# Performance work log

Hardware: AMD Instinct MI355X
Metric: run time of the kernel (lower is better)

Reference implementation:

```python
import jax, jax.numpy as jnp
import numpy as np

B, L, C = 32, 8192, 64
LEVELS = 3  # detail kernels 3,5,9 with pads 1,2,4


def _conv1d(x, w, b, pad):
    # x: [B, C, L], w: [O, I, K] (torch Conv1d layout), b: [O]
    y = jax.lax.conv_general_dilated(
        x, w, window_strides=(1,), padding=[(pad, pad)],
        dimension_numbers=('NCH', 'OIH', 'NCH'))
    return y + b[None, :, None]


def _block(xc, w1, b1, w2, b2, pad):
    # Conv1d(k) -> ReLU -> Conv1d(k=1)
    h = jax.nn.relu(_conv1d(xc, w1, b1, pad))
    return _conv1d(h, w2, b2, 0)


def setup_inputs() -> dict:
    key = jax.random.key(0)
    ks = jax.random.split(key, 20)
    s = 0.05  # keep activations stable
    inp = {
        'x': jax.random.normal(ks[0], (B, L, C), jnp.float32),
        'rec_weights': jnp.ones((LEVELS + 1,), jnp.float32) / (LEVELS + 1),
        'trend_w1': jax.random.normal(ks[1], (C, C, 3), jnp.float32) * s,
        'trend_b1': jnp.zeros((C,), jnp.float32),
        'trend_w2': jax.random.normal(ks[2], (C, C, 1), jnp.float32) * s,
        'trend_b2': jnp.zeros((C,), jnp.float32),
    }
    kernels = [3, 5, 9]
    for i, k in enumerate(kernels, start=1):
        inp[f'd{i}_w1'] = jax.random.normal(ks[2 + 2 * i], (C, C, k), jnp.float32) * s
        inp[f'd{i}_b1'] = jnp.zeros((C,), jnp.float32)
        inp[f'd{i}_w2'] = jax.random.normal(ks[3 + 2 * i], (C, C, 1), jnp.float32) * s
        inp[f'd{i}_b2'] = jnp.zeros((C,), jnp.float32)
    return inp


def reference(x, rec_weights,
              trend_w1, trend_b1, trend_w2, trend_b2,
              d1_w1, d1_b1, d1_w2, d1_b2,
              d2_w1, d2_b1, d2_w2, d2_b2,
              d3_w1, d3_b1, d3_w2, d3_b2):
    # component_fusion forward: x [B, L, C] -> [B, L, C]
    xc = jnp.transpose(x, (0, 2, 1))  # [B, C, L]
    trend = _block(xc, trend_w1, trend_b1, trend_w2, trend_b2, 1)
    d1 = _block(xc, d1_w1, d1_b1, d1_w2, d1_b2, 1)   # k=3, pad=1
    d2 = _block(xc, d2_w1, d2_b1, d2_w2, d2_b2, 2)   # k=5, pad=2
    d3 = _block(xc, d3_w1, d3_b1, d3_w2, d3_b2, 4)   # k=9, pad=4
    w = jax.nn.softmax(rec_weights)
    fused = w[0] * trend + w[1] * d1 + w[2] * d2 + w[3] * d3
    return jnp.transpose(fused, (0, 2, 1))
```

## Files before the change

### kernel.cpp

```cpp
#include <hip/hip_runtime.h>


constexpr int Bn = 32, Ln = 8192;
constexpr int NT = 256;
constexpr int HALO = 4;
constexpr int XROWS = NT + 2 * HALO;
constexpr int RS = 72;
constexpr int NSLICE = 24;

using bf16x8 = __attribute__((ext_vector_type(8))) __bf16;
using f32x4  = __attribute__((ext_vector_type(4))) float;
using u16x8  = __attribute__((ext_vector_type(8))) unsigned short;
using u16x4  = __attribute__((ext_vector_type(4))) unsigned short;
using s16x4  = __attribute__((ext_vector_type(4))) short;

struct Ptrs {
    const float* x;
    const float* rw;
    const float* w1[4];
    const float* b1[4];
    const float* w2[4];
    const float* b2[4];
};

__device__ __forceinline__ unsigned short f2bf(float f) {
    __bf16 h = (__bf16)f;
    return __builtin_bit_cast(unsigned short, h);
}

#if defined(__has_builtin)
#  if __has_builtin(__builtin_amdgcn_mfma_f32_16x16x16bf16_1k)
#    define HAVE_MFMA16 1
#  endif
#endif

__device__ __forceinline__ void mfma16(f32x4& c, u16x4 a, u16x4 b) {
#ifdef HAVE_MFMA16
    c = __builtin_amdgcn_mfma_f32_16x16x16bf16_1k(
            __builtin_bit_cast(s16x4, a), __builtin_bit_cast(s16x4, b), c, 0, 0, 0);
#else
    asm("v_mfma_f32_16x16x16_bf16 %0, %1, %2, %0" : "+v"(c) : "v"(a), "v"(b));
#endif
}

__device__ __forceinline__ void stage_slice(const unsigned short* __restrict__ frag,
                                            unsigned short* wbuf, int s, int tid) {
    const unsigned short* g = frag + (size_t)s * 4096 + tid * 8;
    unsigned short* l = wbuf + (s & 3) * 4096 + tid * 8;
    __builtin_amdgcn_global_load_lds(
        (const __attribute__((address_space(1))) unsigned int*)g,
        (__attribute__((address_space(3))) unsigned int*)l, 16, 0, 0);
    __builtin_amdgcn_global_load_lds(
        (const __attribute__((address_space(1))) unsigned int*)(g + 2048),
        (__attribute__((address_space(3))) unsigned int*)(l + 2048), 16, 0, 0);
}

template <int N>
__device__ __forceinline__ void wait_bar() {
    if constexpr (N == 4)      asm volatile("s_waitcnt vmcnt(4)" ::: "memory");
    else if constexpr (N == 2) asm volatile("s_waitcnt vmcnt(2)" ::: "memory");
    else                       asm volatile("s_waitcnt vmcnt(0)" ::: "memory");
    __builtin_amdgcn_sched_barrier(0);
    __builtin_amdgcn_s_barrier();
    __builtin_amdgcn_sched_barrier(0);
}

__device__ __forceinline__ void wait_bar_for(int S) {
    if (S <= 21)      wait_bar<4>();
    else if (S == 22) wait_bar<2>();
    else              wait_bar<0>();
}

__global__ void prep_kernel(Ptrs p, unsigned short* __restrict__ frag, float* __restrict__ hdr) {
    int tid = threadIdx.x;
    float v0 = p.rw[0], v1 = p.rw[1], v2 = p.rw[2], v3 = p.rw[3];
    float m = fmaxf(fmaxf(v0, v1), fmaxf(v2, v3));
    float e0 = expf(v0 - m), e1 = expf(v1 - m), e2 = expf(v2 - m), e3 = expf(v3 - m);
    float s = e0 + e1 + e2 + e3;
    float w[4] = {e0 / s, e1 / s, e2 / s, e3 / s};

    if (blockIdx.x == 0) {
        if (tid < 4) hdr[tid] = w[tid];
        if (tid < 64) {
            float fb = 0.f;
            #pragma unroll
            for (int i = 0; i < 4; i++) fb += w[i] * p.b2[i][tid];
            hdr[4 + tid] = fb;
        }
    }

    const int kk[4] = {3, 3, 5, 9};
    const int sbase[4] = {0, 4, 8, 14};

    for (int idx = blockIdx.x * blockDim.x + tid; idx < NSLICE * 4096; idx += gridDim.x * blockDim.x) {
        int sl = idx >> 12;
        int e = idx & 4095;
        int br = 3;
        #pragma unroll
        for (int i = 2; i >= 0; i--) if (sl < sbase[i + 1]) br = i;
        int local = sl - sbase[br];
        unsigned short val;
        if (local < kk[br]) {
            int blk = e >> 9;
            int ks = blk >> 2, mt = blk & 3;
            int sub = e & 511;
            int lane = sub >> 3, j = sub & 7;
            int co = mt * 16 + (lane & 15);
            int ci = ks * 32 + (lane >> 4) * 8 + j;
            val = f2bf(p.w1[br][(co * 64 + ci) * kk[br] + local]);
        } else {
            int fi = e >> 8;
            int kb = fi >> 2, mt = fi & 3;
            int sub = e & 255;
            int lane = sub >> 2, j = sub & 3;
            int co = mt * 16 + (lane & 15);
            int ci = kb * 16 + (lane >> 4) * 4 + j;
            val = f2bf(w[br] * p.w2[br][co * 64 + ci]);
        }
        frag[idx] = val;
    }
}

template <int KK, int PP, int S0>
__device__ __forceinline__ void do_branch(const unsigned short* __restrict__ frag,
                                          unsigned short* wbuf,
                                          const float* b1l,
                                          const unsigned short* xs,
                                          int tid, int lane, int wl0,
                                          f32x4 (&fused)[4][4]) {
    int col = lane & 15, kg = lane >> 4;

    f32x4 acc[4][4];
    #pragma unroll
    for (int mt = 0; mt < 4; mt++)
        #pragma unroll
        for (int nt = 0; nt < 4; nt++)
            acc[mt][nt] = f32x4{0.f, 0.f, 0.f, 0.f};

    #pragma unroll
    for (int dk = 0; dk < KK; dk++) {
        const int S = S0 + dk;
        wait_bar_for(S);
        const unsigned short* wb = wbuf + (S & 3) * 4096;
        #pragma unroll
        for (int ks = 0; ks < 2; ks++) {
            bf16x8 bfr[4];
            #pragma unroll
            for (int nt = 0; nt < 4; nt++) {
                int row = wl0 + nt * 16 + col + (HALO - PP) + dk;
                bfr[nt] = __builtin_bit_cast(bf16x8, *(const u16x8*)&xs[row * RS + ks * 32 + kg * 8]);
            }
            #pragma unroll
            for (int mt = 0; mt < 4; mt++) {
                bf16x8 afr = __builtin_bit_cast(bf16x8,
                    *(const u16x8*)(wb + (ks * 4 + mt) * 512 + lane * 8));
                #pragma unroll
                for (int nt = 0; nt < 4; nt++)
                    acc[mt][nt] = __builtin_amdgcn_mfma_f32_16x16x32_bf16(afr, bfr[nt], acc[mt][nt], 0, 0, 0);
            }
        }
        if (S + 3 < NSLICE) stage_slice(frag, wbuf, S + 3, tid);
    }

    constexpr int SF2 = S0 + KK;
    f32x4 bv[4];
    #pragma unroll
    for (int mt = 0; mt < 4; mt++) bv[mt] = *(const f32x4*)&b1l[mt * 16 + kg * 4];

    wait_bar_for(SF2);
    const unsigned short* wb2 = wbuf + (SF2 & 3) * 4096;

    #pragma unroll
    for (int kb = 0; kb < 4; kb++) {
        u16x4 hb[4];
        #pragma unroll
        for (int nt = 0; nt < 4; nt++) {
            u16x4 h;
            #pragma unroll
            for (int r = 0; r < 4; r++) h[r] = f2bf(fmaxf(acc[kb][nt][r] + bv[kb][r], 0.f));
            hb[nt] = h;
        }
        #pragma unroll
        for (int mt = 0; mt < 4; mt++) {
            u16x4 afr = *(const u16x4*)(wb2 + (kb * 4 + mt) * 256 + lane * 4);
            #pragma unroll
            for (int nt = 0; nt < 4; nt++)
                mfma16(fused[mt][nt], afr, hb[nt]);
        }
    }
    if (SF2 + 3 < NSLICE) stage_slice(frag, wbuf, SF2 + 3, tid);
}

__global__ __launch_bounds__(256, 2) void wavelet_main(Ptrs p,
                                                       const unsigned short* __restrict__ frag,
                                                       const float* __restrict__ hdr,
                                                       float* __restrict__ out) {
    __shared__ unsigned short xs[XROWS * RS];
    __shared__ unsigned short wbuf[4 * 4096];
    __shared__ float b1l[4 * 64];
    __shared__ float fbl[64];

    int tid = threadIdx.x;
    int b = blockIdx.x >> 5;
    int t0 = (blockIdx.x & 31) * NT;

    {
        int c0 = (tid & 7) * 8;
        int rbase = tid >> 3;
        #pragma unroll
        for (int it = 0; it < 9; it++) {
            int rr = it * 32 + rbase;
            if (rr < XROWS) {
                int l = t0 + rr - HALO;
                u16x8 v = {0, 0, 0, 0, 0, 0, 0, 0};
                if (l >= 0 && l < Ln) {
                    const float* src = &p.x[((size_t)b * Ln + l) * 64 + c0];
                    f32x4 a0 = *(const f32x4*)src;
                    f32x4 a1 = *(const f32x4*)(src + 4);
                    #pragma unroll
                    for (int r = 0; r < 4; r++) { v[r] = f2bf(a0[r]); v[4 + r] = f2bf(a1[r]); }
                }
                *(u16x8*)&xs[rr * RS + c0] = v;
            }
        }
    }
    b1l[tid] = p.b1[tid >> 6][tid & 63];
    if (tid < 64) fbl[tid] = hdr[4 + tid];
    __builtin_amdgcn_sched_barrier(0);

    stage_slice(frag, wbuf, 0, tid);
    stage_slice(frag, wbuf, 1, tid);
    stage_slice(frag, wbuf, 2, tid);

    asm volatile("s_waitcnt lgkmcnt(0)" ::: "memory");
    __builtin_amdgcn_sched_barrier(0);
    __builtin_amdgcn_s_barrier();
    __builtin_amdgcn_sched_barrier(0);

    int lane = tid & 63;
    int wl0 = (tid >> 6) * 64;
    int kg = lane >> 4;

    f32x4 fused[4][4];
    #pragma unroll
    for (int mt = 0; mt < 4; mt++)
        #pragma unroll
        for (int nt = 0; nt < 4; nt++)
            fused[mt][nt] = f32x4{0.f, 0.f, 0.f, 0.f};

    do_branch<3, 1, 0 >(frag, wbuf, b1l + 0 * 64, xs, tid, lane, wl0, fused);
    do_branch<3, 1, 4 >(frag, wbuf, b1l + 1 * 64, xs, tid, lane, wl0, fused);
    do_branch<5, 2, 8 >(frag, wbuf, b1l + 2 * 64, xs, tid, lane, wl0, fused);
    do_branch<9, 4, 14>(frag, wbuf, b1l + 3 * 64, xs, tid, lane, wl0, fused);

#ifndef HAVE_MFMA16
    asm volatile("s_nop 7\ns_nop 7");
#endif

    int col = lane & 15;
    f32x4 fb[4];
    #pragma unroll
    for (int mt = 0; mt < 4; mt++) fb[mt] = *(const f32x4*)&fbl[mt * 16 + kg * 4];
    #pragma unroll
    for (int mt = 0; mt < 4; mt++) {
        #pragma unroll
        for (int nt = 0; nt < 4; nt++) {
            int l = t0 + wl0 + nt * 16 + col;
            f32x4 v;
            #pragma unroll
            for (int r = 0; r < 4; r++) v[r] = fused[mt][nt][r] + fb[mt][r];
            *(f32x4*)&out[((size_t)b * Ln + l) * 64 + mt * 16 + kg * 4] = v;
        }
    }
}

extern "C" void kernel_launch(void* const* d_in, const int* in_sizes, int n_in,
                              void* d_out, int out_size, void* d_ws, size_t ws_size,
                              hipStream_t stream) {
    Ptrs p;
    p.x  = (const float*)d_in[0];
    p.rw = (const float*)d_in[1];
    for (int i = 0; i < 4; i++) {
        p.w1[i] = (const float*)d_in[2 + 4 * i];
        p.b1[i] = (const float*)d_in[3 + 4 * i];
        p.w2[i] = (const float*)d_in[4 + 4 * i];
        p.b2[i] = (const float*)d_in[5 + 4 * i];
    }
    float* hdr = (float*)d_ws;
    unsigned short* frag = (unsigned short*)((char*)d_ws + 512);

    hipLaunchKernelGGL(prep_kernel, dim3(96), dim3(256), 0, stream, p, frag, hdr);
    hipLaunchKernelGGL(wavelet_main, dim3(Bn * (Ln / NT)), dim3(256), 0, stream, p, frag, hdr,
                       (float*)d_out);
}
```

Baseline: 69.40 us.

## Software-pipeline weight fragments into registers one slice ahead of MFMA use

Restructures the per-branch loop into a compile-time chain of 24 periods, one per weight slice. Each period prefetches the next slice's weight fragments from LDS into a register double buffer (A/B) before running the current slice's MFMAs. The 1x1 weight fragments are re-laid out in the prep kernel so they share the 8-chunk register format, and MFMA blocks are wrapped in s_setprio. The aim is to hide LDS read latency behind MFMA work. The cost is extra VGPR pressure, which could hurt occupancy at the 2-block launch bound.

```diff
diff --git a/kernel.cpp b/kernel.cpp
--- a/kernel.cpp
+++ b/kernel.cpp
@@ -7,6 +7,10 @@
 constexpr int XROWS = NT + 2 * HALO;
 constexpr int RS = 72;
 constexpr int NSLICE = 24;
+
+constexpr int BRS[NSLICE] = {0,0,0,0, 1,1,1,1, 2,2,2,2,2,2, 3,3,3,3,3,3,3,3,3,3};
+constexpr int DKS[NSLICE] = {0,1,2,-1, 0,1,2,-1, 0,1,2,3,4,-1, 0,1,2,3,4,5,6,7,8,-1};
+constexpr int PPB[4] = {1, 1, 2, 4};
 
 using bf16x8 = __attribute__((ext_vector_type(8))) __bf16;
 using f32x4  = __attribute__((ext_vector_type(4))) float;
@@ -53,22 +57,6 @@
     __builtin_amdgcn_global_load_lds(
         (const __attribute__((address_space(1))) unsigned int*)(g + 2048),
         (__attribute__((address_space(3))) unsigned int*)(l + 2048), 16, 0, 0);
-}
-
-template <int N>
-__device__ __forceinline__ void wait_bar() {
-    if constexpr (N == 4)      asm volatile("s_waitcnt vmcnt(4)" ::: "memory");
-    else if constexpr (N == 2) asm volatile("s_waitcnt vmcnt(2)" ::: "memory");
-    else                       asm volatile("s_waitcnt vmcnt(0)" ::: "memory");
-    __builtin_amdgcn_sched_barrier(0);
-    __builtin_amdgcn_s_barrier();
-    __builtin_amdgcn_sched_barrier(0);
-}
-
-__device__ __forceinline__ void wait_bar_for(int S) {
-    if (S <= 21)      wait_bar<4>();
-    else if (S == 22) wait_bar<2>();
-    else              wait_bar<0>();
 }
 
 __global__ void prep_kernel(Ptrs p, unsigned short* __restrict__ frag, float* __restrict__ hdr) {
@@ -109,10 +97,13 @@
             int ci = ks * 32 + (lane >> 4) * 8 + j;
             val = f2bf(p.w1[br][(co * 64 + ci) * kk[br] + local]);
         } else {
-            int fi = e >> 8;
-            int kb = fi >> 2, mt = fi & 3;
-            int sub = e & 255;
-            int lane = sub >> 2, j = sub & 3;
+            int c = e >> 9;
+            int sub = e & 511;
+            int lane = sub >> 3;
+            int rest = sub & 7;
+            int h = rest >> 2, j = rest & 3;
+            int f = c * 2 + h;
+            int kb = f >> 2, mt = f & 3;
             int co = mt * 16 + (lane & 15);
             int ci = kb * 16 + (lane >> 4) * 4 + j;
             val = f2bf(w[br] * p.w2[br][co * 64 + ci]);
@@ -121,27 +112,41 @@
     }
 }
 
-template <int KK, int PP, int S0>
-__device__ __forceinline__ void do_branch(const unsigned short* __restrict__ frag,
-                                          unsigned short* wbuf,
-                                          const float* b1l,
-                                          const unsigned short* xs,
-                                          int tid, int lane, int wl0,
-                                          f32x4 (&fused)[4][4]) {
+template <int S>
+__device__ __forceinline__ void period(const unsigned short* __restrict__ frag,
+                                       unsigned short* wbuf,
+                                       const unsigned short* xs,
+                                       const float* b1l,
+                                       int tid, int lane, int wl0,
+                                       f32x4 (&acc)[4][4], f32x4 (&fused)[4][4],
+                                       bf16x8 (&cur)[8], bf16x8 (&nxt)[8]) {
+    if constexpr (S <= 21) asm volatile("s_waitcnt vmcnt(2)" ::: "memory");
+    else                   asm volatile("s_waitcnt vmcnt(0)" ::: "memory");
+    __builtin_amdgcn_sched_barrier(0);
+    __builtin_amdgcn_s_barrier();
+    __builtin_amdgcn_sched_barrier(0);
+
+    if constexpr (S + 1 < NSLICE) {
+        const unsigned short* nb = wbuf + ((S + 1) & 3) * 4096 + lane * 8;
+        #pragma unroll
+        for (int c = 0; c < 8; c++)
+            nxt[c] = __builtin_bit_cast(bf16x8, *(const u16x8*)(nb + c * 512));
+    }
+    if constexpr (S + 3 < NSLICE) stage_slice(frag, wbuf, S + 3, tid);
+
+    constexpr int br = BRS[S];
+    constexpr int dk = DKS[S];
     int col = lane & 15, kg = lane >> 4;
 
-    f32x4 acc[4][4];
-    #pragma unroll
-    for (int mt = 0; mt < 4; mt++)
-        #pragma unroll
-        for (int nt = 0; nt < 4; nt++)
-            acc[mt][nt] = f32x4{0.f, 0.f, 0.f, 0.f};
-
-    #pragma unroll
-    for (int dk = 0; dk < KK; dk++) {
-        const int S = S0 + dk;
-        wait_bar_for(S);
-        const unsigned short* wb = wbuf + (S & 3) * 4096;
+    if constexpr (dk >= 0) {
+        if constexpr (dk == 0) {
+            #pragma unroll
+            for (int mt = 0; mt < 4; mt++)
+                #pragma unroll
+                for (int nt = 0; nt < 4; nt++)
+                    acc[mt][nt] = f32x4{0.f, 0.f, 0.f, 0.f};
+        }
+        constexpr int PP = PPB[br];
         #pragma unroll
         for (int ks = 0; ks < 2; ks++) {
             bf16x8 bfr[4];
@@ -150,45 +155,56 @@
                 int row = wl0 + nt * 16 + col + (HALO - PP) + dk;
                 bfr[nt] = __builtin_bit_cast(bf16x8, *(const u16x8*)&xs[row * RS + ks * 32 + kg * 8]);
             }
-            #pragma unroll
-            for (int mt = 0; mt < 4; mt++) {
-                bf16x8 afr = __builtin_bit_cast(bf16x8,
-                    *(const u16x8*)(wb + (ks * 4 + mt) * 512 + lane * 8));
+            __builtin_amdgcn_s_setprio(1);
+            #pragma unroll
+            for (int mt = 0; mt < 4; mt++)
                 #pragma unroll
                 for (int nt = 0; nt < 4; nt++)
-                    acc[mt][nt] = __builtin_amdgcn_mfma_f32_16x16x32_bf16(afr, bfr[nt], acc[mt][nt], 0, 0, 0);
+                    acc[mt][nt] = __builtin_amdgcn_mfma_f32_16x16x32_bf16(cur[ks * 4 + mt], bfr[nt], acc[mt][nt], 0, 0, 0);
+            __builtin_amdgcn_s_setprio(0);
+        }
+    } else {
+        const float* bb = b1l + br * 64;
+        f32x4 bv[4];
+        #pragma unroll
+        for (int mt = 0; mt < 4; mt++) bv[mt] = *(const f32x4*)&bb[mt * 16 + kg * 4];
+        #pragma unroll
+        for (int kb = 0; kb < 4; kb++) {
+            u16x4 hb[4];
+            #pragma unroll
+            for (int nt = 0; nt < 4; nt++) {
+                u16x4 h;
+                #pragma unroll
+                for (int r = 0; r < 4; r++) h[r] = f2bf(fmaxf(acc[kb][nt][r] + bv[kb][r], 0.f));
+                hb[nt] = h;
             }
-        }
-        if (S + 3 < NSLICE) stage_slice(frag, wbuf, S + 3, tid);
-    }
-
-    constexpr int SF2 = S0 + KK;
-    f32x4 bv[4];
-    #pragma unroll
-    for (int mt = 0; mt < 4; mt++) bv[mt] = *(const f32x4*)&b1l[mt * 16 + kg * 4];
-
-    wait_bar_for(SF2);
-    const unsigned short* wb2 = wbuf + (SF2 & 3) * 4096;
-
-    #pragma unroll
-    for (int kb = 0; kb < 4; kb++) {
-        u16x4 hb[4];
-        #pragma unroll
-        for (int nt = 0; nt < 4; nt++) {
-            u16x4 h;
-            #pragma unroll
-            for (int r = 0; r < 4; r++) h[r] = f2bf(fmaxf(acc[kb][nt][r] + bv[kb][r], 0.f));
-            hb[nt] = h;
-        }
-        #pragma unroll
-        for (int mt = 0; mt < 4; mt++) {
-            u16x4 afr = *(const u16x4*)(wb2 + (kb * 4 + mt) * 256 + lane * 4);
-            #pragma unroll
-            for (int nt = 0; nt < 4; nt++)
-                mfma16(fused[mt][nt], afr, hb[nt]);
-        }
-    }
-    if (SF2 + 3 < NSLICE) stage_slice(frag, wbuf, SF2 + 3, tid);
+            __builtin_amdgcn_s_setprio(1);
+            #pragma unroll
+            for (int mt2 = 0; mt2 < 4; mt2++) {
+                constexpr int dummy = 0; (void)dummy;
+                int f = kb * 4 + mt2;
+                u16x8 u = __builtin_bit_cast(u16x8, cur[f >> 1]);
+                int h4 = (f & 1) * 4;
+                u16x4 afr = {u[h4], u[h4 + 1], u[h4 + 2], u[h4 + 3]};
+                #pragma unroll
+                for (int nt = 0; nt < 4; nt++)
+                    mfma16(fused[mt2][nt], afr, hb[nt]);
+            }
+            __builtin_amdgcn_s_setprio(0);
+        }
+    }
+}
+
+template <int S>
+__device__ __forceinline__ void chain(const unsigned short* __restrict__ frag,
+                                      unsigned short* wbuf, const unsigned short* xs,
+                                      const float* b1l, int tid, int lane, int wl0,
+                                      f32x4 (&acc)[4][4], f32x4 (&fused)[4][4],
+                                      bf16x8 (&A)[8], bf16x8 (&B)[8]) {
+    if constexpr (S & 1) period<S>(frag, wbuf, xs, b1l, tid, lane, wl0, acc, fused, B, A);
+    else                 period<S>(frag, wbuf, xs, b1l, tid, lane, wl0, acc, fused, A, B);
+    if constexpr (S + 1 < NSLICE)
+        chain<S + 1>(frag, wbuf, xs, b1l, tid, lane, wl0, acc, fused, A, B);
 }
 
 __global__ __launch_bounds__(256, 2) void wavelet_main(Ptrs p,
@@ -232,7 +248,7 @@
     stage_slice(frag, wbuf, 1, tid);
     stage_slice(frag, wbuf, 2, tid);
 
-    asm volatile("s_waitcnt lgkmcnt(0)" ::: "memory");
+    asm volatile("s_waitcnt vmcnt(4) lgkmcnt(0)" ::: "memory");
     __builtin_amdgcn_sched_barrier(0);
     __builtin_amdgcn_s_barrier();
     __builtin_amdgcn_sched_barrier(0);
@@ -241,6 +257,15 @@
     int wl0 = (tid >> 6) * 64;
     int kg = lane >> 4;
 
+    bf16x8 A[8], B[8];
+    {
+        const unsigned short* b0 = wbuf + lane * 8;
+        #pragma unroll
+        for (int c = 0; c < 8; c++)
+            A[c] = __builtin_bit_cast(bf16x8, *(const u16x8*)(b0 + c * 512));
+    }
+
+    f32x4 acc[4][4];
     f32x4 fused[4][4];
     #pragma unroll
     for (int mt = 0; mt < 4; mt++)
@@ -248,10 +273,7 @@
         for (int nt = 0; nt < 4; nt++)
             fused[mt][nt] = f32x4{0.f, 0.f, 0.f, 0.f};
 
-    do_branch<3, 1, 0 >(frag, wbuf, b1l + 0 * 64, xs, tid, lane, wl0, fused);
-    do_branch<3, 1, 4 >(frag, wbuf, b1l + 1 * 64, xs, tid, lane, wl0, fused);
-    do_branch<5, 2, 8 >(frag, wbuf, b1l + 2 * 64, xs, tid, lane, wl0, fused);
-    do_branch<9, 4, 14>(frag, wbuf, b1l + 3 * 64, xs, tid, lane, wl0, fused);
+    chain<0>(frag, wbuf, xs, b1l, tid, lane, wl0, acc, fused, A, B);
 
 #ifndef HAVE_MFMA16
     asm volatile("s_nop 7\ns_nop 7");
@@ -262,10 +284,10 @@
     #pragma unroll
     for (int mt = 0; mt < 4; mt++) fb[mt] = *(const f32x4*)&fbl[mt * 16 + kg * 4];
     #pragma unroll
-    for (int mt = 0; mt < 4; mt++) {
-        #pragma unroll
-        for (int nt = 0; nt < 4; nt++) {
-            int l = t0 + wl0 + nt * 16 + col;
+    for (int nt = 0; nt < 4; nt++) {
+        int l = t0 + wl0 + nt * 16 + col;
+        #pragma unroll
+        for (int mt = 0; mt < 4; mt++) {
             f32x4 v;
             #pragma unroll
             for (int r = 0; r < 4; r++) v[r] = fused[mt][nt][r] + fb[mt][r];
```

Measured after the change: 68.33 us. No clear change (-1.5%).
